# Performance work log

Measured on AMD Instinct MI355X. Metric: run time of the kernel, lower is better.

## Reference

```python
import jax, jax.numpy as jnp
import numpy as np

USR_SIZE = 100000
EMB = 64
BATCH = 4096
HIST = 200


def setup_inputs() -> dict:
    key = jax.random.key(0)
    k1, k2 = jax.random.split(key)
    # USERLIST as stored by the module: np.append(-1, param.USERLIST), sorted ids
    userlist = jnp.concatenate([jnp.array([-1], dtype=jnp.int64),
                                jnp.arange(USR_SIZE, dtype=jnp.int64)])
    x = jax.random.randint(k1, (BATCH, HIST), 0, USR_SIZE, dtype=jnp.int64)
    emb_usr = jax.random.normal(k2, (USR_SIZE + 1, EMB), dtype=jnp.float32)
    return {"x": x, "userlist": userlist, "emb_usr": emb_usr}


def reference(x, userlist, emb_usr):
    # Equivalent to per-element np.where(USERLIST == u)[0][0]: USERLIST is
    # sorted and every u appears exactly once, so searchsorted gives the
    # same index as the linear scan. Then a single embedding gather.
    usr2id = jnp.searchsorted(userlist, x)  # [B, L]
    return emb_usr[usr2id]                  # [B, L, EMB]
```

## Files before the change

### kernel.cpp

```cpp
#include <hip/hip_runtime.h>
#include <hip/hip_bf16.h>
#include <limits.h>


#define V4_PER_ROW 16
#define ELEMS_PER_BLOCK 2048
#define NXCD 8

typedef float f32x4 __attribute__((ext_vector_type(4)));
typedef int   i32x4 __attribute__((ext_vector_type(4)));

__device__ __forceinline__ void store_stream_f4(f32x4* p, f32x4 v)
{
    asm volatile("global_store_dwordx4 %0, %1, off nt sc0 sc1"
                 :
                 : "v"(p), "v"(v));
}

__device__ __forceinline__ i32x4 load_stream_i4(const int* p)
{
    i32x4 r;
    asm volatile("global_load_dwordx4 %0, %1, off nt sc0 sc1\n\t"
                 "s_waitcnt vmcnt(0)"
                 : "=v"(r)
                 : "v"(p));
    return r;
}

__global__ __launch_bounds__(256) void usr_emb_gather(
    const int* __restrict__ x,
    const int* __restrict__ userlist, int n_user,
    const float* __restrict__ emb,
    float* __restrict__ out,
    int n_elem)
{
    __shared__ int q_id[ELEMS_PER_BLOCK];
    __shared__ int q_ge[ELEMS_PER_BLOCK];
    __shared__ int q_count;

    const int t    = threadIdx.x;
    const int lane = t & 63;
    const int wave = t >> 6;

    const int c  = blockIdx.x & (NXCD - 1);
    const int j  = blockIdx.x >> 3;
    const int e0 = j * ELEMS_PER_BLOCK;

    const int rs    = (n_user + NXCD - 1) >> 3;
    const int lo_id = c * rs;
    const int hi_id = min(lo_id + rs, n_user);

    if (t == 0) q_count = 0;
    __syncthreads();

    const int ul_lo = (lo_id > 0) ? userlist[lo_id - 1] : INT_MIN;
    const int ul_hi = userlist[hi_id - 1];
    const int v1    = userlist[1];

#pragma unroll
    for (int r = 0; r < 2; ++r) {
        const int base = e0 + r * 1024 + t * 4;
        int  u[4];
        bool valid[4];
        if (base + 3 < n_elem) {
            const i32x4 xv = load_stream_i4(x + base);
            u[0] = xv.x; u[1] = xv.y; u[2] = xv.z; u[3] = xv.w;
            valid[0] = valid[1] = valid[2] = valid[3] = true;
        } else {
#pragma unroll
            for (int k = 0; k < 4; ++k) {
                valid[k] = (base + k) < n_elem;
                u[k]     = valid[k] ? x[base + k] : 0;
            }
        }
#pragma unroll
        for (int k = 0; k < 4; ++k) {
            const bool flag = valid[k]
                              && (lo_id == 0 || u[k] > ul_lo)
                              && (u[k] <= ul_hi);
            int id = 0;
            if (flag) {
                int g = 1 + (u[k] - v1);
                bool hit = (g >= 1 && g < n_user) && (userlist[g] == u[k]);
                if (!hit) {
                    int lo = 0, hi = n_user;
                    while (lo < hi) {
                        const int mid = (lo + hi) >> 1;
                        if (userlist[mid] < u[k]) lo = mid + 1;
                        else                      hi = mid;
                    }
                    g = lo;
                }
                id = g;
            }
            const unsigned long long m = __ballot(flag);
            if (m) {
                int pos = 0;
                if (lane == 0) pos = atomicAdd(&q_count, __popcll(m));
                pos = __shfl(pos, 0);
                pos += __popcll(m & ((1ull << lane) - 1ull));
                if (flag) {
                    q_id[pos] = id;
                    q_ge[pos] = base + k;
                }
            }
        }
    }
    __syncthreads();

    const int count = q_count;
    const f32x4* __restrict__ emb4 = (const f32x4*)emb;
    f32x4*       __restrict__ out4 = (f32x4*)out;

    const int sub   = lane & (V4_PER_ROW - 1);
    const int eslot = lane >> 4;

    for (int i = wave * 4 + eslot; i < count; i += 16) {
        const int id = q_id[i];
        const int ge = q_ge[i];
        const f32x4 row = emb4[(size_t)id * V4_PER_ROW + sub];
        store_stream_f4(&out4[(size_t)ge * V4_PER_ROW + sub], row);
    }
}

extern "C" void kernel_launch(void* const* d_in, const int* in_sizes, int n_in,
                              void* d_out, int out_size, void* d_ws, size_t ws_size,
                              hipStream_t stream) {
    const int*   x        = (const int*)d_in[0];
    const int*   userlist = (const int*)d_in[1];
    const float* emb      = (const float*)d_in[2];
    float*       out      = (float*)d_out;

    const int n_elem = in_sizes[0];
    const int n_user = in_sizes[1];

    const int chunks = (n_elem + ELEMS_PER_BLOCK - 1) / ELEMS_PER_BLOCK;
    const int blocks = chunks * NXCD;
    usr_emb_gather<<<blocks, 256, 0, stream>>>(x, userlist, n_user, emb, out, n_elem);
}
```

Baseline: 264.4 us.

## Use hardware XCC id and atomic work-stealing to bind id-ranges to XCDs

Before, the XCD partition was taken from blockIdx, assuming blocks are dealt round-robin to XCDs. Now each block reads its real XCC id from a hardware register and claims chunks from per-partition atomic counters, starting with its own XCD's id range and then stealing from the others. The aim is to keep each embedding slice in the L2 of the XCD that serves it, even when block placement is not round-robin. This adds global atomics, extra block-wide barriers per chunk, and a memset launch to clear the counters.

```diff
diff --git a/kernel.cpp b/kernel.cpp
--- a/kernel.cpp
+++ b/kernel.cpp
@@ -1,5 +1,4 @@
 #include <hip/hip_runtime.h>
-#include <hip/hip_bf16.h>
 #include <limits.h>
 
 
@@ -27,99 +26,118 @@
     return r;
 }
 
+__device__ __forceinline__ int get_xcc_id()
+{
+    int v;
+    asm("s_getreg_b32 %0, hwreg(20, 0, 32)" : "=s"(v));
+    return v & (NXCD - 1);
+}
+
 __global__ __launch_bounds__(256) void usr_emb_gather(
     const int* __restrict__ x,
     const int* __restrict__ userlist, int n_user,
     const float* __restrict__ emb,
     float* __restrict__ out,
-    int n_elem)
+    int n_elem, int n_chunks,
+    int* __restrict__ claim)
 {
     __shared__ int q_id[ELEMS_PER_BLOCK];
     __shared__ int q_ge[ELEMS_PER_BLOCK];
     __shared__ int q_count;
+    __shared__ int s_j;
 
     const int t    = threadIdx.x;
     const int lane = t & 63;
     const int wave = t >> 6;
 
-    const int c  = blockIdx.x & (NXCD - 1);
-    const int j  = blockIdx.x >> 3;
-    const int e0 = j * ELEMS_PER_BLOCK;
+    const int xcd = get_xcc_id();
+    const int rs  = (n_user + NXCD - 1) >> 3;
 
-    const int rs    = (n_user + NXCD - 1) >> 3;
-    const int lo_id = c * rs;
-    const int hi_id = min(lo_id + rs, n_user);
-
-    if (t == 0) q_count = 0;
-    __syncthreads();
-
-    const int ul_lo = (lo_id > 0) ? userlist[lo_id - 1] : INT_MIN;
-    const int ul_hi = userlist[hi_id - 1];
-    const int v1    = userlist[1];
-
-#pragma unroll
-    for (int r = 0; r < 2; ++r) {
-        const int base = e0 + r * 1024 + t * 4;
-        int  u[4];
-        bool valid[4];
-        if (base + 3 < n_elem) {
-            const i32x4 xv = load_stream_i4(x + base);
-            u[0] = xv.x; u[1] = xv.y; u[2] = xv.z; u[3] = xv.w;
-            valid[0] = valid[1] = valid[2] = valid[3] = true;
-        } else {
-#pragma unroll
-            for (int k = 0; k < 4; ++k) {
-                valid[k] = (base + k) < n_elem;
-                u[k]     = valid[k] ? x[base + k] : 0;
-            }
-        }
-#pragma unroll
-        for (int k = 0; k < 4; ++k) {
-            const bool flag = valid[k]
-                              && (lo_id == 0 || u[k] > ul_lo)
-                              && (u[k] <= ul_hi);
-            int id = 0;
-            if (flag) {
-                int g = 1 + (u[k] - v1);
-                bool hit = (g >= 1 && g < n_user) && (userlist[g] == u[k]);
-                if (!hit) {
-                    int lo = 0, hi = n_user;
-                    while (lo < hi) {
-                        const int mid = (lo + hi) >> 1;
-                        if (userlist[mid] < u[k]) lo = mid + 1;
-                        else                      hi = mid;
-                    }
-                    g = lo;
-                }
-                id = g;
-            }
-            const unsigned long long m = __ballot(flag);
-            if (m) {
-                int pos = 0;
-                if (lane == 0) pos = atomicAdd(&q_count, __popcll(m));
-                pos = __shfl(pos, 0);
-                pos += __popcll(m & ((1ull << lane) - 1ull));
-                if (flag) {
-                    q_id[pos] = id;
-                    q_ge[pos] = base + k;
-                }
-            }
-        }
-    }
-    __syncthreads();
-
-    const int count = q_count;
     const f32x4* __restrict__ emb4 = (const f32x4*)emb;
     f32x4*       __restrict__ out4 = (f32x4*)out;
-
     const int sub   = lane & (V4_PER_ROW - 1);
     const int eslot = lane >> 4;
 
-    for (int i = wave * 4 + eslot; i < count; i += 16) {
-        const int id = q_id[i];
-        const int ge = q_ge[i];
-        const f32x4 row = emb4[(size_t)id * V4_PER_ROW + sub];
-        store_stream_f4(&out4[(size_t)ge * V4_PER_ROW + sub], row);
+    const int v1 = userlist[1];
+
+    for (int cc = 0; cc < NXCD; ++cc) {
+        const int c     = (xcd + cc) & (NXCD - 1);
+        const int lo_id = c * rs;
+        const int hi_id = min(lo_id + rs, n_user);
+        const int ul_lo = (lo_id > 0) ? userlist[lo_id - 1] : INT_MIN;
+        const int ul_hi = userlist[hi_id - 1];
+
+        for (;;) {
+            if (t == 0) {
+                s_j     = atomicAdd(&claim[c], 1);
+                q_count = 0;
+            }
+            __syncthreads();
+            const int j = s_j;
+            if (j >= n_chunks) break;
+            const int e0 = j * ELEMS_PER_BLOCK;
+
+#pragma unroll
+            for (int r = 0; r < 2; ++r) {
+                const int base = e0 + r * 1024 + t * 4;
+                int  u[4];
+                bool valid[4];
+                if (base + 3 < n_elem) {
+                    const i32x4 xv = load_stream_i4(x + base);
+                    u[0] = xv.x; u[1] = xv.y; u[2] = xv.z; u[3] = xv.w;
+                    valid[0] = valid[1] = valid[2] = valid[3] = true;
+                } else {
+#pragma unroll
+                    for (int k = 0; k < 4; ++k) {
+                        valid[k] = (base + k) < n_elem;
+                        u[k]     = valid[k] ? x[base + k] : 0;
+                    }
+                }
+#pragma unroll
+                for (int k = 0; k < 4; ++k) {
+                    const bool flag = valid[k]
+                                      && (lo_id == 0 || u[k] > ul_lo)
+                                      && (u[k] <= ul_hi);
+                    int id = 0;
+                    if (flag) {
+                        int g = 1 + (u[k] - v1);
+                        bool hit = (g >= 1 && g < n_user) && (userlist[g] == u[k]);
+                        if (!hit) {
+                            int lo = 0, hi = n_user;
+                            while (lo < hi) {
+                                const int mid = (lo + hi) >> 1;
+                                if (userlist[mid] < u[k]) lo = mid + 1;
+                                else                      hi = mid;
+                            }
+                            g = lo;
+                        }
+                        id = g;
+                    }
+                    const unsigned long long m = __ballot(flag);
+                    if (m) {
+                        int pos = 0;
+                        if (lane == 0) pos = atomicAdd(&q_count, __popcll(m));
+                        pos = __shfl(pos, 0);
+                        pos += __popcll(m & ((1ull << lane) - 1ull));
+                        if (flag) {
+                            q_id[pos] = id;
+                            q_ge[pos] = base + k;
+                        }
+                    }
+                }
+            }
+            __syncthreads();
+
+            const int count = q_count;
+            for (int i = wave * 4 + eslot; i < count; i += 16) {
+                const int id = q_id[i];
+                const int ge = q_ge[i];
+                const f32x4 row = emb4[(size_t)id * V4_PER_ROW + sub];
+                store_stream_f4(&out4[(size_t)ge * V4_PER_ROW + sub], row);
+            }
+            __syncthreads();
+        }
+        __syncthreads();
     }
 }
 
@@ -136,5 +154,8 @@
 
     const int chunks = (n_elem + ELEMS_PER_BLOCK - 1) / ELEMS_PER_BLOCK;
     const int blocks = chunks * NXCD;
-    usr_emb_gather<<<blocks, 256, 0, stream>>>(x, userlist, n_user, emb, out, n_elem);
+
+    hipMemsetAsync(d_ws, 0, NXCD * sizeof(int), stream);
+    usr_emb_gather<<<blocks, 256, 0, stream>>>(x, userlist, n_user, emb, out,
+                                               n_elem, chunks, (int*)d_ws);
 }
```

After: 551.8 us. +108.7%, slower.
